# Kernel tuning notes

Measured on AMD Instinct MI355X. Metric: run time of the kernel, lower is better.

The kernel has to match this reference:

```python
import jax, jax.numpy as jnp
import numpy as np

N_HEADS = 8
TANH_CLIP = 10.0


def setup_inputs() -> dict:
    key = jax.random.key(0)
    ks = jax.random.split(key, 7)
    B, N, D = 128, 1000, 512
    embeddings = jax.random.normal(ks[0], (B, N, D), dtype=jnp.float32)
    step_context = jax.random.normal(ks[1], (B, 1, 2 * D), dtype=jnp.float32)
    # action mask: True = feasible action; guarantee at least one feasible per row
    action_mask = jax.random.uniform(ks[2], (B, 1, N)) > 0.3
    action_mask = action_mask.at[:, :, 0].set(True)
    s = 0.02
    W_node = jax.random.normal(ks[3], (D, 3 * D), dtype=jnp.float32) * s
    W_fixed = jax.random.normal(ks[4], (D, D), dtype=jnp.float32) * s
    W_step = jax.random.normal(ks[5], (2 * D, D), dtype=jnp.float32) * s
    W_out = jax.random.normal(ks[6], (D, D), dtype=jnp.float32) * s
    return {"embeddings": embeddings, "step_context": step_context,
            "action_mask": action_mask, "W_node": W_node, "W_fixed": W_fixed,
            "W_step": W_step, "W_out": W_out}


def reference(embeddings, step_context, action_mask, W_node, W_fixed, W_step, W_out):
    B, N, D = embeddings.shape
    H = N_HEADS
    hd = D // H
    neg_inf = jnp.float32(-jnp.inf)

    # --- precompute (Decoder._precompute) ---
    graph_embed = embeddings.mean(axis=1)                      # [B, D]
    kvl = embeddings @ W_node                                  # [B, N, 3D]
    _gk, gv, logit_key = jnp.split(kvl, 3, axis=-1)
    # source bug: glimpse_key variable is overwritten with glimpse_val, and
    # attention is called with key = value = glimpse_val
    KV = gv.reshape(B, N, H, hd).transpose(0, 2, 1, 3)         # [B, H, N, hd]
    graph_context = (graph_embed @ W_fixed)[:, None, :]        # [B, 1, D]

    # --- per-step query (Decoder._get_log_p) ---
    query = graph_context + step_context @ W_step              # [B, 1, D]
    q = query.reshape(B, 1, H, hd).transpose(0, 2, 1, 3)       # [B, H, 1, hd]

    # --- inner MHA (scaled_dot_product_attention with boolean mask) ---
    scores = jnp.einsum('bhqs,bhns->bhqn', q, KV) / jnp.sqrt(jnp.float32(hd))
    scores = jnp.where(action_mask[:, None, :, :], scores, neg_inf)  # [B,H,1,N]
    attn = jax.nn.softmax(scores, axis=-1)
    heads = jnp.einsum('bhqn,bhns->bhqs', attn, KV)            # [B, H, 1, hd]
    heads = heads.transpose(0, 2, 1, 3).reshape(B, 1, D)       # [B, 1, D]

    # --- glimpse projection and logit head ---
    glimpse = heads @ W_out                                    # [B, 1, D]
    logits = jnp.einsum('bqd,bnd->bqn', glimpse, logit_key) / jnp.sqrt(jnp.float32(D))
    logits = jnp.tanh(logits) * TANH_CLIP
    logits = jnp.where(action_mask, logits, neg_inf)
    return jax.nn.log_softmax(logits, axis=-1)                 # [B, 1, N]
```

## Files before the change

kernel.cpp:

```cpp
#include <hip/hip_runtime.h>
#include <math.h>

#define B 128
#define N 1000
#define D 512
#define H 8
#define HD 64
#define NCHUNK 8
#define CHUNK 125

#define OFF_PMEAN   0
#define OFF_QW      (OFF_PMEAN + B*NCHUNK*D)
#define OFF_SCORES  (OFF_QW + B*D*H)
#define OFF_PAE     (OFF_SCORES + B*H*N)
#define OFF_GW      (OFF_PAE + B*NCHUNK*H*D)
#define OFF_LOGITS  (OFF_GW + B*D)

__device__ inline float waveMax(float v){
    #pragma unroll
    for (int o = 32; o > 0; o >>= 1) v = fmaxf(v, __shfl_xor(v, o));
    return v;
}
__device__ inline float waveSum(float v){
    #pragma unroll
    for (int o = 32; o > 0; o >>= 1) v += __shfl_xor(v, o);
    return v;
}

__global__ void k1_partial_mean(const float* __restrict__ emb, float* __restrict__ ws){
    int chunk = blockIdx.x, b = blockIdx.y, t = threadIdx.x;
    const float4* e4 = (const float4*)emb;
    float4 acc = make_float4(0.f, 0.f, 0.f, 0.f);
    size_t rowbase = ((size_t)b * N + (size_t)chunk * CHUNK) * (D / 4);
    for (int n = 0; n < CHUNK; ++n) {
        float4 v = e4[rowbase + (size_t)n * (D / 4) + t];
        acc.x += v.x; acc.y += v.y; acc.z += v.z; acc.w += v.w;
    }
    float4* o = (float4*)(ws + OFF_PMEAN + (size_t)(b * NCHUNK + chunk) * D);
    o[t] = acc;
}

__global__ void k2_prep(const float* __restrict__ stepc, const float* __restrict__ Wnode,
                        const float* __restrict__ Wfix, const float* __restrict__ Wstep,
                        float* __restrict__ ws){
    int b = blockIdx.x, d = threadIdx.x;
    __shared__ float ge[D];
    __shared__ float q[D];
    float s = 0.f;
    for (int c = 0; c < NCHUNK; ++c) s += ws[OFF_PMEAN + (size_t)(b * NCHUNK + c) * D + d];
    ge[d] = s * (1.0f / N);
    __syncthreads();
    float acc = 0.f;
    for (int k = 0; k < D; ++k) acc = fmaf(ge[k], Wfix[(size_t)k * D + d], acc);
    const float* sc = stepc + (size_t)b * 2 * D;
    for (int k = 0; k < 2 * D; ++k) acc = fmaf(sc[k], Wstep[(size_t)k * D + d], acc);
    q[d] = acc;
    __syncthreads();
    const float* wrow = Wnode + (size_t)d * 3 * D + D;
    float* outp = ws + OFF_QW + ((size_t)b * D + d) * H;
    #pragma unroll
    for (int h = 0; h < H; ++h) {
        float a = 0.f;
        const float* qh = q + h * HD;
        const float* wh = wrow + h * HD;
        for (int s2 = 0; s2 < HD; ++s2) a = fmaf(qh[s2], wh[s2], a);
        outp[h] = a;
    }
}

__global__ void k3_scores(const float* __restrict__ emb, const unsigned char* __restrict__ mask,
                          float* __restrict__ ws){
    int chunk = blockIdx.x, b = blockIdx.y, t = threadIdx.x;
    __shared__ float4 qw4[D * H / 4];
    const float4* qg = (const float4*)(ws + OFF_QW + (size_t)b * D * H);
    #pragma unroll
    for (int i = 0; i < 8; ++i) qw4[i * 128 + t] = qg[i * 128 + t];
    __syncthreads();
    if (t >= CHUNK) return;
    int n = chunk * CHUNK + t;
    const float4* e4 = (const float4*)(emb + ((size_t)b * N + n) * D);
    float acc[H];
    #pragma unroll
    for (int h = 0; h < H; ++h) acc[h] = 0.f;
    for (int d4 = 0; d4 < D / 4; ++d4) {
        float4 e = e4[d4];
        #pragma unroll
        for (int j = 0; j < 4; ++j) {
            int d = d4 * 4 + j;
            float4 a = qw4[d * 2];
            float4 c = qw4[d * 2 + 1];
            float ev = (j == 0) ? e.x : (j == 1) ? e.y : (j == 2) ? e.z : e.w;
            acc[0] = fmaf(ev, a.x, acc[0]); acc[1] = fmaf(ev, a.y, acc[1]);
            acc[2] = fmaf(ev, a.z, acc[2]); acc[3] = fmaf(ev, a.w, acc[3]);
            acc[4] = fmaf(ev, c.x, acc[4]); acc[5] = fmaf(ev, c.y, acc[5]);
            acc[6] = fmaf(ev, c.z, acc[6]); acc[7] = fmaf(ev, c.w, acc[7]);
        }
    }
    bool m = mask[(size_t)b * N + n] != 0;
    const float scl = 0.125f;
    #pragma unroll
    for (int h = 0; h < H; ++h) {
        float v = m ? acc[h] * scl : -INFINITY;
        ws[OFF_SCORES + ((size_t)(b * H + h)) * N + n] = v;
    }
}

__global__ void k4_softmax(float* __restrict__ ws){
    int row = blockIdx.x, t = threadIdx.x;
    float* s = ws + OFF_SCORES + (size_t)row * N;
    float v[4];
    float mx = -INFINITY;
    #pragma unroll
    for (int k = 0; k < 4; ++k) {
        int j = t + k * 256;
        v[k] = (j < N) ? s[j] : -INFINITY;
        mx = fmaxf(mx, v[k]);
    }
    __shared__ float red[4], red2[4];
    mx = waveMax(mx);
    int wid = t >> 6, lane = t & 63;
    if (lane == 0) red[wid] = mx;
    __syncthreads();
    mx = fmaxf(fmaxf(red[0], red[1]), fmaxf(red[2], red[3]));
    float sum = 0.f;
    #pragma unroll
    for (int k = 0; k < 4; ++k) { v[k] = expf(v[k] - mx); sum += v[k]; }
    sum = waveSum(sum);
    if (lane == 0) red2[wid] = sum;
    __syncthreads();
    sum = red2[0] + red2[1] + red2[2] + red2[3];
    float inv = 1.0f / sum;
    #pragma unroll
    for (int k = 0; k < 4; ++k) { int j = t + k * 256; if (j < N) s[j] = v[k] * inv; }
}

__global__ void k5_pae(const float* __restrict__ emb, float* __restrict__ ws){
    int chunk = blockIdx.x, b = blockIdx.y, t = threadIdx.x;
    __shared__ float attn[H * CHUNK];
    for (int f = t; f < H * CHUNK; f += 512) {
        int h = f / CHUNK, i = f % CHUNK;
        attn[f] = ws[OFF_SCORES + ((size_t)(b * H + h)) * N + chunk * CHUNK + i];
    }
    __syncthreads();
    float acc[H];
    #pragma unroll
    for (int h = 0; h < H; ++h) acc[h] = 0.f;
    const float* eb = emb + ((size_t)b * N + (size_t)chunk * CHUNK) * D + t;
    for (int i = 0; i < CHUNK; ++i) {
        float e = eb[(size_t)i * D];
        #pragma unroll
        for (int h = 0; h < H; ++h) acc[h] = fmaf(attn[h * CHUNK + i], e, acc[h]);
    }
    #pragma unroll
    for (int h = 0; h < H; ++h)
        ws[OFF_PAE + (((size_t)(b * NCHUNK + chunk)) * H + h) * D + t] = acc[h];
}

__global__ void k6_post(const float* __restrict__ Wnode, const float* __restrict__ Wout,
                        float* __restrict__ ws){
    int b = blockIdx.x, t = threadIdx.x;
    __shared__ float ae[H * D];
    __shared__ float heads[D];
    __shared__ float gl[D];
    #pragma unroll
    for (int h = 0; h < H; ++h) {
        float s = 0.f;
        for (int c = 0; c < NCHUNK; ++c)
            s += ws[OFF_PAE + (((size_t)(b * NCHUNK + c)) * H + h) * D + t];
        ae[h * D + t] = s;
    }
    __syncthreads();
    {
        int h = t >> 6, s2 = t & 63;
        float a = 0.f;
        const float* col = Wnode + D + h * HD + s2;
        const float* aeh = ae + h * D;
        for (int d = 0; d < D; ++d) a = fmaf(aeh[d], col[(size_t)d * 3 * D], a);
        heads[t] = a;
    }
    __syncthreads();
    {
        float a = 0.f;
        for (int d = 0; d < D; ++d) a = fmaf(heads[d], Wout[(size_t)d * D + t], a);
        gl[t] = a;
    }
    __syncthreads();
    {
        float a = 0.f;
        const float* wrow = Wnode + (size_t)t * 3 * D + 2 * D;
        for (int e = 0; e < D; ++e) a = fmaf(gl[e], wrow[e], a);
        ws[OFF_GW + (size_t)b * D + t] = a;
    }
}

__global__ void k7_logits(const float* __restrict__ emb, const unsigned char* __restrict__ mask,
                          float* __restrict__ ws){
    int chunk = blockIdx.x, b = blockIdx.y, t = threadIdx.x;
    __shared__ float4 gw4[D / 4];
    const float4* gg = (const float4*)(ws + OFF_GW + (size_t)b * D);
    gw4[t] = gg[t];
    __syncthreads();
    if (t >= CHUNK) return;
    int n = chunk * CHUNK + t;
    const float4* e4 = (const float4*)(emb + ((size_t)b * N + n) * D);
    float acc = 0.f;
    for (int d4 = 0; d4 < D / 4; ++d4) {
        float4 e = e4[d4];
        float4 g = gw4[d4];
        acc = fmaf(e.x, g.x, acc); acc = fmaf(e.y, g.y, acc);
        acc = fmaf(e.z, g.z, acc); acc = fmaf(e.w, g.w, acc);
    }
    float lg = tanhf(acc * 0.044194173824159216f) * 10.0f;
    bool m = mask[(size_t)b * N + n] != 0;
    ws[OFF_LOGITS + (size_t)b * N + n] = m ? lg : -INFINITY;
}

__global__ void k8_logsoftmax(const float* __restrict__ ws, float* __restrict__ out){
    int b = blockIdx.x, t = threadIdx.x;
    const float* lg = ws + OFF_LOGITS + (size_t)b * N;
    float v[4];
    float mx = -INFINITY;
    #pragma unroll
    for (int k = 0; k < 4; ++k) {
        int j = t + k * 256;
        v[k] = (j < N) ? lg[j] : -INFINITY;
        mx = fmaxf(mx, v[k]);
    }
    __shared__ float red[4], red2[4];
    mx = waveMax(mx);
    int wid = t >> 6, lane = t & 63;
    if (lane == 0) red[wid] = mx;
    __syncthreads();
    mx = fmaxf(fmaxf(red[0], red[1]), fmaxf(red[2], red[3]));
    float sum = 0.f;
    #pragma unroll
    for (int k = 0; k < 4; ++k) sum += expf(v[k] - mx);
    sum = waveSum(sum);
    if (lane == 0) red2[wid] = sum;
    __syncthreads();
    sum = red2[0] + red2[1] + red2[2] + red2[3];
    float L = mx + logf(sum);
    #pragma unroll
    for (int k = 0; k < 4; ++k) {
        int j = t + k * 256;
        if (j < N) {
            float r = v[k] - L;
            out[(size_t)b * N + j] = fmaxf(r, -1e30f);
        }
    }
}

extern "C" void kernel_launch(void* const* d_in, const int* in_sizes, int n_in,
                              void* d_out, int out_size, void* d_ws, size_t ws_size,
                              hipStream_t stream) {
    const float* emb   = (const float*)d_in[0];
    const float* stepc = (const float*)d_in[1];
    const unsigned char* mask = (const unsigned char*)d_in[2];
    const float* Wnode = (const float*)d_in[3];
    const float* Wfix  = (const float*)d_in[4];
    const float* Wstep = (const float*)d_in[5];
    const float* Wout  = (const float*)d_in[6];
    float* out = (float*)d_out;
    float* ws  = (float*)d_ws;

    k1_partial_mean<<<dim3(NCHUNK, B), 128, 0, stream>>>(emb, ws);
    k2_prep<<<dim3(B), 512, 0, stream>>>(stepc, Wnode, Wfix, Wstep, ws);
    k3_scores<<<dim3(NCHUNK, B), 128, 0, stream>>>(emb, mask, ws);
    k4_softmax<<<dim3(B * H), 256, 0, stream>>>(ws);
    k5_pae<<<dim3(NCHUNK, B), 512, 0, stream>>>(emb, ws);
    k6_post<<<dim3(B), 512, 0, stream>>>(Wnode, Wout, ws);
    k7_logits<<<dim3(NCHUNK, B), 128, 0, stream>>>(emb, mask, ws);
    k8_logsoftmax<<<dim3(B), 256, 0, stream>>>(ws, out);
}
```

Measured before the change: 358.9 us.

## Fuse scores, softmax and weighted sum into one flash-style attention kernel

Merges the score, softmax and attention-weighted-sum kernels into a single kernel that stages embedding sub-tiles in shared memory and keeps an online softmax (running max and sum), so embeddings are read once for both the scores and the weighted sum. Partial results per chunk group are combined with max-rescaling in the post kernel. It also folds the per-chunk max and sum of the logit log-softmax into the logits kernel, and splits dot-product loops across multiple accumulators. This removes one full pass over the embeddings and two kernel launches, at the cost of more synchronisation and shared-memory use per block.

```diff
diff --git a/kernel.cpp b/kernel.cpp
--- a/kernel.cpp
+++ b/kernel.cpp
@@ -5,27 +5,22 @@
 #define N 1000
 #define D 512
 #define H 8
-#define HD 64
 #define NCHUNK 8
 #define CHUNK 125
+#define CG_N 10
+#define SUBR 25
+#define NSUB 4
+#define ESW 516
 
 #define OFF_PMEAN   0
 #define OFF_QW      (OFF_PMEAN + B*NCHUNK*D)
-#define OFF_SCORES  (OFF_QW + B*D*H)
-#define OFF_PAE     (OFF_SCORES + B*H*N)
-#define OFF_GW      (OFF_PAE + B*NCHUNK*H*D)
-#define OFF_LOGITS  (OFF_GW + B*D)
-
-__device__ inline float waveMax(float v){
-    #pragma unroll
-    for (int o = 32; o > 0; o >>= 1) v = fmaxf(v, __shfl_xor(v, o));
-    return v;
-}
-__device__ inline float waveSum(float v){
-    #pragma unroll
-    for (int o = 32; o > 0; o >>= 1) v += __shfl_xor(v, o);
-    return v;
-}
+#define OFF_PAE     (OFF_QW + B*D*H)
+#define OFF_MC      (OFF_PAE + B*CG_N*H*D)
+#define OFF_ZC      (OFF_MC + B*CG_N*H)
+#define OFF_GW      (OFF_ZC + B*CG_N*H)
+#define OFF_LG      (OFF_GW + B*D)
+#define OFF_LMAX    (OFF_LG + B*N)
+#define OFF_LSUM    (OFF_LMAX + B*NCHUNK)
 
 __global__ void k1_partial_mean(const float* __restrict__ emb, float* __restrict__ ws){
     int chunk = blockIdx.x, b = blockIdx.y, t = threadIdx.x;
@@ -47,149 +42,206 @@
     __shared__ float ge[D];
     __shared__ float q[D];
     float s = 0.f;
+    #pragma unroll
     for (int c = 0; c < NCHUNK; ++c) s += ws[OFF_PMEAN + (size_t)(b * NCHUNK + c) * D + d];
     ge[d] = s * (1.0f / N);
     __syncthreads();
-    float acc = 0.f;
-    for (int k = 0; k < D; ++k) acc = fmaf(ge[k], Wfix[(size_t)k * D + d], acc);
+    float a0 = 0.f, a1 = 0.f, a2 = 0.f, a3 = 0.f;
+    for (int k = 0; k < D; k += 4) {
+        a0 = fmaf(ge[k],     Wfix[(size_t)k * D + d],       a0);
+        a1 = fmaf(ge[k + 1], Wfix[(size_t)(k + 1) * D + d], a1);
+        a2 = fmaf(ge[k + 2], Wfix[(size_t)(k + 2) * D + d], a2);
+        a3 = fmaf(ge[k + 3], Wfix[(size_t)(k + 3) * D + d], a3);
+    }
     const float* sc = stepc + (size_t)b * 2 * D;
-    for (int k = 0; k < 2 * D; ++k) acc = fmaf(sc[k], Wstep[(size_t)k * D + d], acc);
-    q[d] = acc;
+    for (int k = 0; k < 2 * D; k += 4) {
+        a0 = fmaf(sc[k],     Wstep[(size_t)k * D + d],       a0);
+        a1 = fmaf(sc[k + 1], Wstep[(size_t)(k + 1) * D + d], a1);
+        a2 = fmaf(sc[k + 2], Wstep[(size_t)(k + 2) * D + d], a2);
+        a3 = fmaf(sc[k + 3], Wstep[(size_t)(k + 3) * D + d], a3);
+    }
+    q[d] = (a0 + a1) + (a2 + a3);
     __syncthreads();
     const float* wrow = Wnode + (size_t)d * 3 * D + D;
     float* outp = ws + OFF_QW + ((size_t)b * D + d) * H;
     #pragma unroll
     for (int h = 0; h < H; ++h) {
         float a = 0.f;
-        const float* qh = q + h * HD;
-        const float* wh = wrow + h * HD;
-        for (int s2 = 0; s2 < HD; ++s2) a = fmaf(qh[s2], wh[s2], a);
+        const float* qh = q + h * 64;
+        const float* wh = wrow + h * 64;
+        #pragma unroll 8
+        for (int s2 = 0; s2 < 64; ++s2) a = fmaf(qh[s2], wh[s2], a);
         outp[h] = a;
     }
 }
 
-__global__ void k3_scores(const float* __restrict__ emb, const unsigned char* __restrict__ mask,
-                          float* __restrict__ ws){
-    int chunk = blockIdx.x, b = blockIdx.y, t = threadIdx.x;
-    __shared__ float4 qw4[D * H / 4];
-    const float4* qg = (const float4*)(ws + OFF_QW + (size_t)b * D * H);
-    #pragma unroll
-    for (int i = 0; i < 8; ++i) qw4[i * 128 + t] = qg[i * 128 + t];
-    __syncthreads();
-    if (t >= CHUNK) return;
-    int n = chunk * CHUNK + t;
-    const float4* e4 = (const float4*)(emb + ((size_t)b * N + n) * D);
+__global__ __launch_bounds__(512) void kc_attn(const float* __restrict__ emb,
+        const unsigned char* __restrict__ mask, float* __restrict__ ws){
+    const int cg = blockIdx.x, b = blockIdx.y, t = threadIdx.x;
+    __shared__ float es[SUBR * ESW];
+    __shared__ float ps[16 * H * 32];
+    __shared__ float sc[H * 32];
+    __shared__ float pp[H * 32];
+    __shared__ float mrun[H], zrun[H], ff[H];
     float acc[H];
     #pragma unroll
     for (int h = 0; h < H; ++h) acc[h] = 0.f;
-    for (int d4 = 0; d4 < D / 4; ++d4) {
-        float4 e = e4[d4];
-        #pragma unroll
-        for (int j = 0; j < 4; ++j) {
-            int d = d4 * 4 + j;
-            float4 a = qw4[d * 2];
-            float4 c = qw4[d * 2 + 1];
-            float ev = (j == 0) ? e.x : (j == 1) ? e.y : (j == 2) ? e.z : e.w;
-            acc[0] = fmaf(ev, a.x, acc[0]); acc[1] = fmaf(ev, a.y, acc[1]);
-            acc[2] = fmaf(ev, a.z, acc[2]); acc[3] = fmaf(ev, a.w, acc[3]);
-            acc[4] = fmaf(ev, c.x, acc[4]); acc[5] = fmaf(ev, c.y, acc[5]);
-            acc[6] = fmaf(ev, c.z, acc[6]); acc[7] = fmaf(ev, c.w, acc[7]);
-        }
-    }
-    bool m = mask[(size_t)b * N + n] != 0;
-    const float scl = 0.125f;
-    #pragma unroll
-    for (int h = 0; h < H; ++h) {
-        float v = m ? acc[h] * scl : -INFINITY;
-        ws[OFF_SCORES + ((size_t)(b * H + h)) * N + n] = v;
-    }
-}
-
-__global__ void k4_softmax(float* __restrict__ ws){
-    int row = blockIdx.x, t = threadIdx.x;
-    float* s = ws + OFF_SCORES + (size_t)row * N;
-    float v[4];
-    float mx = -INFINITY;
-    #pragma unroll
-    for (int k = 0; k < 4; ++k) {
-        int j = t + k * 256;
-        v[k] = (j < N) ? s[j] : -INFINITY;
-        mx = fmaxf(mx, v[k]);
-    }
-    __shared__ float red[4], red2[4];
-    mx = waveMax(mx);
-    int wid = t >> 6, lane = t & 63;
-    if (lane == 0) red[wid] = mx;
-    __syncthreads();
-    mx = fmaxf(fmaxf(red[0], red[1]), fmaxf(red[2], red[3]));
-    float sum = 0.f;
-    #pragma unroll
-    for (int k = 0; k < 4; ++k) { v[k] = expf(v[k] - mx); sum += v[k]; }
-    sum = waveSum(sum);
-    if (lane == 0) red2[wid] = sum;
-    __syncthreads();
-    sum = red2[0] + red2[1] + red2[2] + red2[3];
-    float inv = 1.0f / sum;
-    #pragma unroll
-    for (int k = 0; k < 4; ++k) { int j = t + k * 256; if (j < N) s[j] = v[k] * inv; }
-}
-
-__global__ void k5_pae(const float* __restrict__ emb, float* __restrict__ ws){
-    int chunk = blockIdx.x, b = blockIdx.y, t = threadIdx.x;
-    __shared__ float attn[H * CHUNK];
-    for (int f = t; f < H * CHUNK; f += 512) {
-        int h = f / CHUNK, i = f % CHUNK;
-        attn[f] = ws[OFF_SCORES + ((size_t)(b * H + h)) * N + chunk * CHUNK + i];
-    }
-    __syncthreads();
-    float acc[H];
-    #pragma unroll
-    for (int h = 0; h < H; ++h) acc[h] = 0.f;
-    const float* eb = emb + ((size_t)b * N + (size_t)chunk * CHUNK) * D + t;
-    for (int i = 0; i < CHUNK; ++i) {
-        float e = eb[(size_t)i * D];
-        #pragma unroll
-        for (int h = 0; h < H; ++h) acc[h] = fmaf(attn[h * CHUNK + i], e, acc[h]);
-    }
-    #pragma unroll
-    for (int h = 0; h < H; ++h)
-        ws[OFF_PAE + (((size_t)(b * NCHUNK + chunk)) * H + h) * D + t] = acc[h];
-}
-
-__global__ void k6_post(const float* __restrict__ Wnode, const float* __restrict__ Wout,
-                        float* __restrict__ ws){
+    if (t < H) { mrun[t] = -INFINITY; zrun[t] = 0.f; }
+    __syncthreads();
+    const float* qw = ws + OFF_QW + (size_t)b * D * H;
+    const int n_b = t & 31, dblk = t >> 5;
+    for (int sub = 0; sub < NSUB; ++sub) {
+        const int row0 = cg * (NSUB * SUBR) + sub * SUBR;
+        const float4* e4 = (const float4*)(emb + ((size_t)b * N + row0) * D);
+        #pragma unroll
+        for (int r = 0; r < 7; ++r) {
+            int idx = r * 512 + t;
+            if (idx < SUBR * (D / 4)) {
+                float4 v = e4[idx];
+                int i = idx >> 7, c = idx & 127;
+                *(float4*)&es[i * ESW + c * 4] = v;
+            }
+        }
+        __syncthreads();
+        {
+            float a[H];
+            #pragma unroll
+            for (int h = 0; h < H; ++h) a[h] = 0.f;
+            if (n_b < SUBR) {
+                const float* er = es + n_b * ESW + dblk * 32;
+                const float* qd = qw + (size_t)(dblk * 32) * H;
+                #pragma unroll 8
+                for (int dd = 0; dd < 32; ++dd) {
+                    float e = er[dd];
+                    float4 q0 = *(const float4*)(qd + dd * 8);
+                    float4 q1 = *(const float4*)(qd + dd * 8 + 4);
+                    a[0] = fmaf(e, q0.x, a[0]); a[1] = fmaf(e, q0.y, a[1]);
+                    a[2] = fmaf(e, q0.z, a[2]); a[3] = fmaf(e, q0.w, a[3]);
+                    a[4] = fmaf(e, q1.x, a[4]); a[5] = fmaf(e, q1.y, a[5]);
+                    a[6] = fmaf(e, q1.z, a[6]); a[7] = fmaf(e, q1.w, a[7]);
+                }
+            }
+            #pragma unroll
+            for (int h = 0; h < H; ++h) ps[(dblk * H + h) * 32 + n_b] = a[h];
+        }
+        __syncthreads();
+        if (t < 256) {
+            int h = t >> 5, n = t & 31;
+            float s = -INFINITY;
+            if (n < SUBR) {
+                float v = 0.f;
+                #pragma unroll
+                for (int k = 0; k < 16; ++k) v += ps[(k * H + h) * 32 + n];
+                bool m = mask[(size_t)b * N + row0 + n] != 0;
+                s = m ? v * 0.125f : -INFINITY;
+            }
+            sc[h * 32 + n] = s;
+        }
+        __syncthreads();
+        if (t < 256) {
+            int h = t >> 5, j = t & 31;
+            float v = sc[h * 32 + j];
+            float gm = v;
+            #pragma unroll
+            for (int o = 16; o > 0; o >>= 1) gm = fmaxf(gm, __shfl_xor(gm, o));
+            float mold = mrun[h];
+            float mnew = fmaxf(mold, gm);
+            float p = (mnew == -INFINITY) ? 0.f : __expf(v - mnew);
+            pp[h * 32 + j] = p;
+            float zc = p;
+            #pragma unroll
+            for (int o = 16; o > 0; o >>= 1) zc += __shfl_xor(zc, o);
+            if (j == 0) {
+                float f = (mnew == -INFINITY) ? 1.f : __expf(mold - mnew);
+                ff[h] = f;
+                mrun[h] = mnew;
+                zrun[h] = zrun[h] * f + zc;
+            }
+        }
+        __syncthreads();
+        #pragma unroll
+        for (int h = 0; h < H; ++h) acc[h] *= ff[h];
+        for (int i = 0; i < SUBR; ++i) {
+            float e = es[i * ESW + t];
+            #pragma unroll
+            for (int h = 0; h < H; ++h) acc[h] = fmaf(pp[h * 32 + i], e, acc[h]);
+        }
+        __syncthreads();
+    }
+    float* paeb = ws + OFF_PAE + (((size_t)b * CG_N + cg) * H) * (size_t)D;
+    #pragma unroll
+    for (int h = 0; h < H; ++h) paeb[(size_t)h * D + t] = acc[h];
+    if (t < H) {
+        ws[OFF_MC + ((size_t)b * CG_N + cg) * H + t] = mrun[t];
+        ws[OFF_ZC + ((size_t)b * CG_N + cg) * H + t] = zrun[t];
+    }
+}
+
+__global__ __launch_bounds__(512) void kd_post(const float* __restrict__ Wnode,
+        const float* __restrict__ Wout, float* __restrict__ ws){
     int b = blockIdx.x, t = threadIdx.x;
     __shared__ float ae[H * D];
     __shared__ float heads[D];
     __shared__ float gl[D];
+    __shared__ float wgt[CG_N * H], iZ[H];
+    if (t < H) {
+        float M = -INFINITY;
+        for (int c = 0; c < CG_N; ++c)
+            M = fmaxf(M, ws[OFF_MC + ((size_t)b * CG_N + c) * H + t]);
+        float Z = 0.f;
+        for (int c = 0; c < CG_N; ++c) {
+            float m = ws[OFF_MC + ((size_t)b * CG_N + c) * H + t];
+            float w = (m == -INFINITY) ? 0.f : __expf(m - M);
+            wgt[c * H + t] = w;
+            Z += w * ws[OFF_ZC + ((size_t)b * CG_N + c) * H + t];
+        }
+        iZ[t] = 1.0f / Z;
+    }
+    __syncthreads();
     #pragma unroll
     for (int h = 0; h < H; ++h) {
         float s = 0.f;
-        for (int c = 0; c < NCHUNK; ++c)
-            s += ws[OFF_PAE + (((size_t)(b * NCHUNK + c)) * H + h) * D + t];
-        ae[h * D + t] = s;
+        #pragma unroll
+        for (int c = 0; c < CG_N; ++c)
+            s += wgt[c * H + h] * ws[OFF_PAE + (((size_t)b * CG_N + c) * H + h) * (size_t)D + t];
+        ae[h * D + t] = s * iZ[h];
     }
     __syncthreads();
     {
-        int h = t >> 6, s2 = t & 63;
-        float a = 0.f;
-        const float* col = Wnode + D + h * HD + s2;
+        int h = t >> 6;
         const float* aeh = ae + h * D;
-        for (int d = 0; d < D; ++d) a = fmaf(aeh[d], col[(size_t)d * 3 * D], a);
-        heads[t] = a;
+        const float* col = Wnode + 512 + t;
+        float a0 = 0.f, a1 = 0.f, a2 = 0.f, a3 = 0.f;
+        for (int d = 0; d < D; d += 4) {
+            a0 = fmaf(aeh[d],     col[(size_t)d * (3 * D)],       a0);
+            a1 = fmaf(aeh[d + 1], col[(size_t)(d + 1) * (3 * D)], a1);
+            a2 = fmaf(aeh[d + 2], col[(size_t)(d + 2) * (3 * D)], a2);
+            a3 = fmaf(aeh[d + 3], col[(size_t)(d + 3) * (3 * D)], a3);
+        }
+        heads[t] = (a0 + a1) + (a2 + a3);
     }
     __syncthreads();
     {
-        float a = 0.f;
-        for (int d = 0; d < D; ++d) a = fmaf(heads[d], Wout[(size_t)d * D + t], a);
-        gl[t] = a;
+        float a0 = 0.f, a1 = 0.f, a2 = 0.f, a3 = 0.f;
+        for (int d = 0; d < D; d += 4) {
+            a0 = fmaf(heads[d],     Wout[(size_t)d * D + t],       a0);
+            a1 = fmaf(heads[d + 1], Wout[(size_t)(d + 1) * D + t], a1);
+            a2 = fmaf(heads[d + 2], Wout[(size_t)(d + 2) * D + t], a2);
+            a3 = fmaf(heads[d + 3], Wout[(size_t)(d + 3) * D + t], a3);
+        }
+        gl[t] = (a0 + a1) + (a2 + a3);
     }
     __syncthreads();
     {
-        float a = 0.f;
-        const float* wrow = Wnode + (size_t)t * 3 * D + 2 * D;
-        for (int e = 0; e < D; ++e) a = fmaf(gl[e], wrow[e], a);
-        ws[OFF_GW + (size_t)b * D + t] = a;
+        const float* wrow = Wnode + (size_t)t * (3 * D) + 2 * D;
+        float a0 = 0.f, a1 = 0.f, a2 = 0.f, a3 = 0.f;
+        for (int e = 0; e < D; e += 4) {
+            a0 = fmaf(gl[e],     wrow[e],     a0);
+            a1 = fmaf(gl[e + 1], wrow[e + 1], a1);
+            a2 = fmaf(gl[e + 2], wrow[e + 2], a2);
+            a3 = fmaf(gl[e + 3], wrow[e + 3], a3);
+        }
+        ws[OFF_GW + (size_t)b * D + t] = (a0 + a1) + (a2 + a3);
     }
 }
 
@@ -197,57 +249,62 @@
                           float* __restrict__ ws){
     int chunk = blockIdx.x, b = blockIdx.y, t = threadIdx.x;
     __shared__ float4 gw4[D / 4];
-    const float4* gg = (const float4*)(ws + OFF_GW + (size_t)b * D);
-    gw4[t] = gg[t];
-    __syncthreads();
-    if (t >= CHUNK) return;
+    __shared__ float rmax[2], rsum[2];
+    gw4[t] = ((const float4*)(ws + OFF_GW + (size_t)b * D))[t];
+    __syncthreads();
+    float lg = -INFINITY;
     int n = chunk * CHUNK + t;
-    const float4* e4 = (const float4*)(emb + ((size_t)b * N + n) * D);
-    float acc = 0.f;
-    for (int d4 = 0; d4 < D / 4; ++d4) {
-        float4 e = e4[d4];
-        float4 g = gw4[d4];
-        acc = fmaf(e.x, g.x, acc); acc = fmaf(e.y, g.y, acc);
-        acc = fmaf(e.z, g.z, acc); acc = fmaf(e.w, g.w, acc);
-    }
-    float lg = tanhf(acc * 0.044194173824159216f) * 10.0f;
-    bool m = mask[(size_t)b * N + n] != 0;
-    ws[OFF_LOGITS + (size_t)b * N + n] = m ? lg : -INFINITY;
-}
-
-__global__ void k8_logsoftmax(const float* __restrict__ ws, float* __restrict__ out){
+    if (t < CHUNK) {
+        const float4* e4 = (const float4*)(emb + ((size_t)b * N + n) * D);
+        float a0 = 0.f, a1 = 0.f, a2 = 0.f, a3 = 0.f;
+        for (int d4 = 0; d4 < D / 4; ++d4) {
+            float4 e = e4[d4];
+            float4 g = gw4[d4];
+            a0 = fmaf(e.x, g.x, a0); a1 = fmaf(e.y, g.y, a1);
+            a2 = fmaf(e.z, g.z, a2); a3 = fmaf(e.w, g.w, a3);
+        }
+        float accv = (a0 + a1) + (a2 + a3);
+        bool m = mask[(size_t)b * N + n] != 0;
+        lg = m ? tanhf(accv * 0.044194173824159216f) * 10.0f : -INFINITY;
+        ws[OFF_LG + (size_t)b * N + n] = lg;
+    }
+    float mx = lg;
+    #pragma unroll
+    for (int o = 32; o > 0; o >>= 1) mx = fmaxf(mx, __shfl_xor(mx, o));
+    if ((t & 63) == 0) rmax[t >> 6] = mx;
+    __syncthreads();
+    float bm = fmaxf(rmax[0], rmax[1]);
+    float term = (lg == -INFINITY) ? 0.f : __expf(lg - bm);
+    #pragma unroll
+    for (int o = 32; o > 0; o >>= 1) term += __shfl_xor(term, o);
+    if ((t & 63) == 0) rsum[t >> 6] = term;
+    __syncthreads();
+    if (t == 0) {
+        ws[OFF_LMAX + (size_t)b * NCHUNK + chunk] = bm;
+        ws[OFF_LSUM + (size_t)b * NCHUNK + chunk] = rsum[0] + rsum[1];
+    }
+}
+
+__global__ void k8_out(const float* __restrict__ ws, float* __restrict__ out){
     int b = blockIdx.x, t = threadIdx.x;
-    const float* lg = ws + OFF_LOGITS + (size_t)b * N;
-    float v[4];
-    float mx = -INFINITY;
-    #pragma unroll
-    for (int k = 0; k < 4; ++k) {
-        int j = t + k * 256;
-        v[k] = (j < N) ? lg[j] : -INFINITY;
-        mx = fmaxf(mx, v[k]);
-    }
-    __shared__ float red[4], red2[4];
-    mx = waveMax(mx);
-    int wid = t >> 6, lane = t & 63;
-    if (lane == 0) red[wid] = mx;
-    __syncthreads();
-    mx = fmaxf(fmaxf(red[0], red[1]), fmaxf(red[2], red[3]));
-    float sum = 0.f;
-    #pragma unroll
-    for (int k = 0; k < 4; ++k) sum += expf(v[k] - mx);
-    sum = waveSum(sum);
-    if (lane == 0) red2[wid] = sum;
-    __syncthreads();
-    sum = red2[0] + red2[1] + red2[2] + red2[3];
-    float L = mx + logf(sum);
-    #pragma unroll
-    for (int k = 0; k < 4; ++k) {
-        int j = t + k * 256;
-        if (j < N) {
-            float r = v[k] - L;
-            out[(size_t)b * N + j] = fmaxf(r, -1e30f);
-        }
-    }
+    __shared__ float Ls;
+    if (t == 0) {
+        float M = -INFINITY;
+        #pragma unroll
+        for (int c = 0; c < NCHUNK; ++c)
+            M = fmaxf(M, ws[OFF_LMAX + (size_t)b * NCHUNK + c]);
+        float S = 0.f;
+        #pragma unroll
+        for (int c = 0; c < NCHUNK; ++c) {
+            float m = ws[OFF_LMAX + (size_t)b * NCHUNK + c];
+            if (m != -INFINITY) S += __expf(m - M) * ws[OFF_LSUM + (size_t)b * NCHUNK + c];
+        }
+        Ls = M + __logf(S);
+    }
+    __syncthreads();
+    float L = Ls;
+    for (int j = t; j < N; j += 256)
+        out[(size_t)b * N + j] = fmaxf(ws[OFF_LG + (size_t)b * N + j] - L, -1e30f);
 }
 
 extern "C" void kernel_launch(void* const* d_in, const int* in_sizes, int n_in,
@@ -265,10 +322,8 @@
 
     k1_partial_mean<<<dim3(NCHUNK, B), 128, 0, stream>>>(emb, ws);
     k2_prep<<<dim3(B), 512, 0, stream>>>(stepc, Wnode, Wfix, Wstep, ws);
-    k3_scores<<<dim3(NCHUNK, B), 128, 0, stream>>>(emb, mask, ws);
-    k4_softmax<<<dim3(B * H), 256, 0, stream>>>(ws);
-    k5_pae<<<dim3(NCHUNK, B), 512, 0, stream>>>(emb, ws);
-    k6_post<<<dim3(B), 512, 0, stream>>>(Wnode, Wout, ws);
+    kc_attn<<<dim3(CG_N, B), 512, 0, stream>>>(emb, mask, ws);
+    kd_post<<<dim3(B), 512, 0, stream>>>(Wnode, Wout, ws);
     k7_logits<<<dim3(NCHUNK, B), 128, 0, stream>>>(emb, mask, ws);
-    k8_logsoftmax<<<dim3(B), 256, 0, stream>>>(ws, out);
-}
+    k8_out<<<dim3(B), 256, 0, stream>>>(ws, out);
+}
```

New measurement: 418.8 us. 16.7% more time.
